# Performance work log

Measured on AMD Instinct MI355X. Metric: run time of the kernel, lower is better.

The kernel has to match this reference:

```python
import jax, jax.numpy as jnp
import numpy as np

TEMPERATURE = 8.0  # sqrt(d_k) with d_k=64
NEG = -9e15        # matches torch zero_vec constant -9000000000000000.0


def setup_inputs() -> dict:
    key = jax.random.key(0)
    k1, k2, k3, k4 = jax.random.split(key, 4)
    a, b, N, d = 32, 4, 1024, 64  # a = nhead*b, nhead = 8
    q = jax.random.normal(k1, (a, N, d), dtype=jnp.float32)
    k = jax.random.normal(k2, (a, N, d), dtype=jnp.float32)
    v = jax.random.normal(k3, (a, N, d), dtype=jnp.float32)
    adj = jax.random.randint(k4, (b, N, N), 0, 2, dtype=jnp.int32)
    return {"q": q, "k": k, "v": v, "adj": adj}


def reference(q, k, v, adj):
    # q,k,v: [nhead*b, N, d]; adj: [b, N, N]
    a, N, d = v.shape
    b = adj.shape[0]
    nhead = a // b
    # scores: [a, N, N]
    attn = jnp.einsum('bnd,bmd->bnm', q, k) / jnp.asarray(TEMPERATURE, q.dtype)
    # 'local' focus: mask by adjacency, broadcast over heads (head-major layout
    # matches torch's adj.unsqueeze(0).repeat(nhead,1,1,1).view(-1,N,N))
    attn = attn.reshape(nhead, b, N, N)
    attn = jnp.where(adj[None] > 0, attn, jnp.asarray(NEG, attn.dtype))
    attn = attn.reshape(a, N, N)
    attn = jax.nn.softmax(attn, axis=2)
    # dropout p=0.0 -> identity
    output = jnp.einsum('bnm,bmd->bnd', attn, v)
    return (output, attn)
```

## Files before the change

kernel.cpp:

```cpp
#include <hip/hip_runtime.h>
#include <hip/hip_bf16.h>

#define A_TOT 32
#define SEQ 1024
#define DIM 64
#define NT 16
#define GSTRIDE 1056
#define TILEB (8 * GSTRIDE)

typedef __attribute__((ext_vector_type(8))) short short8;
typedef __attribute__((ext_vector_type(4))) float f32x4;
typedef unsigned long long u64;

static __device__ __forceinline__ unsigned pack2bf(float a, float b) {
    union { __hip_bfloat16 h[2]; unsigned u; } x;
    x.h[0] = __float2bfloat16(a);
    x.h[1] = __float2bfloat16(b);
    return x.u;
}

static __device__ __forceinline__ void gload_lds16(const void* g, void* l) {
    __builtin_amdgcn_global_load_lds(
        (const __attribute__((address_space(1))) unsigned*)g,
        (__attribute__((address_space(3))) unsigned*)l, 16, 0, 0);
}

static __device__ __forceinline__ short8 lds_frag(const unsigned char* tile,
                                                  int row, int chunk) {
    const int byte = (row >> 3) * GSTRIDE + (row & 7) * 128 +
                     ((chunk ^ (row & 7)) << 4);
    return *reinterpret_cast<const short8*>(tile + byte);
}

#define WAITBAR(N) do {                                          \
    asm volatile("s_waitcnt vmcnt(" #N ")" ::: "memory");        \
    __builtin_amdgcn_sched_barrier(0);                           \
    __builtin_amdgcn_s_barrier();                                \
    __builtin_amdgcn_sched_barrier(0);                           \
    asm volatile("" ::: "memory");                               \
} while (0)

__global__ void prepass_kernel(const float* __restrict__ q,
                               const float* __restrict__ k,
                               const float* __restrict__ v,
                               const int* __restrict__ adj,
                               __hip_bfloat16* __restrict__ qb,
                               __hip_bfloat16* __restrict__ kb,
                               __hip_bfloat16* __restrict__ vt,
                               u64* __restrict__ adjm) {
    __shared__ __hip_bfloat16 tile[64][65];
    const int tid = threadIdx.x;
    if (blockIdx.y < 2) {
        const float* src = blockIdx.y ? k : q;
        __hip_bfloat16* dst = blockIdx.y ? kb : qb;
        int i = (blockIdx.x * 256 + tid) * 4;
        float4 f = *reinterpret_cast<const float4*>(src + i);
        union { __hip_bfloat16 h[4]; ushort4 u; } cv;
        cv.h[0] = __float2bfloat16(f.x);
        cv.h[1] = __float2bfloat16(f.y);
        cv.h[2] = __float2bfloat16(f.z);
        cv.h[3] = __float2bfloat16(f.w);
        *reinterpret_cast<ushort4*>(dst + i) = cv.u;
        return;
    }
    if (blockIdx.x < 512) {
        const int bh = blockIdx.x >> 4;
        const int n0 = (blockIdx.x & 15) * 64;
        const float* vsrc = v + ((size_t)bh * SEQ + n0) * DIM;
        for (int e = tid; e < 64 * 64; e += 256) {
            int i = e >> 6;
            int d = e & 63;
            tile[i][d] = __float2bfloat16(vsrc[(size_t)i * DIM + d]);
        }
        __syncthreads();
        __hip_bfloat16* vdst = vt + (size_t)bh * DIM * SEQ + n0;
        for (int e = tid; e < 64 * 64; e += 256) {
            int d = e >> 6;
            int i = e & 63;
            vdst[(size_t)d * SEQ + i] = tile[i][d];
        }
        return;
    }
    if (blockIdx.x < 1536) {
        const int px   = blockIdx.x - 512;
        const int wv   = tid >> 6;
        const int lane = tid & 63;
        const int wbase = px * 64 + wv * 16;
        for (int it = 0; it < 16; ++it) {
            const int w = wbase + it;
            const int a = adj[(size_t)w * 64 + lane];
            u64 m = __ballot(a > 0);
            if (lane == 0) adjm[w] = m;
        }
    }
}

__launch_bounds__(256)
__global__ void graph_attn_kernel(const __hip_bfloat16* __restrict__ qb,
                                  const __hip_bfloat16* __restrict__ kb,
                                  const __hip_bfloat16* __restrict__ vt,
                                  const u64* __restrict__ adjm,
                                  float* __restrict__ out,
                                  float* __restrict__ attn) {
    __shared__ __align__(16) unsigned char kstage[2][TILEB];
    __shared__ __align__(16) unsigned char vstage[2][TILEB];
    __shared__ float part[4][4][16];
    __shared__ float lsum_sh[4][16];

    const int wg    = (blockIdx.x & 7) * 64 + (blockIdx.x >> 3);
    const int bh    = wg >> 4;
    const int rb    = wg & 15;
    const int batch = bh & 3;
    const int tid   = threadIdx.x;
    const int wid   = tid >> 6;
    const int lane  = tid & 63;
    const int lr    = lane & 15;
    const int lgi   = lane >> 4;
    const int row16 = rb * 64 + wid * 16;

    const int sub  = lane >> 3;
    const int csrc = (lane & 7) ^ sub;

    const __hip_bfloat16* qrow = qb + ((size_t)bh * SEQ + row16 + lr) * DIM + lgi * 8;
    const short8 qf0 = *reinterpret_cast<const short8*>(qrow);
    const short8 qf1 = *reinterpret_cast<const short8*>(qrow + 32);

    const u64* mrow = adjm + ((size_t)batch * SEQ + row16 + lr) * (SEQ / 64);
    const __hip_bfloat16* kbh = kb + (size_t)bh * SEQ * DIM;
    const __hip_bfloat16* vth = vt + (size_t)bh * DIM * SEQ;

    const int kperm = (lr >> 2) * 8 + (lr & 3);

    auto stageK = [&](int t, int b) {
        const __hip_bfloat16* g0 = kbh + (size_t)(t * 64 + wid * 16) * DIM;
        unsigned char* l0 = &kstage[b][(wid * 2) * GSTRIDE];
        gload_lds16(g0 + (size_t)sub * DIM + csrc * 8, l0);
        gload_lds16(g0 + (size_t)(8 + sub) * DIM + csrc * 8, l0 + GSTRIDE);
    };
    auto stageV = [&](int t, int b) {
        const __hip_bfloat16* g0 = vth + (size_t)(wid * 16) * SEQ + t * 64;
        unsigned char* l0 = &vstage[b][(wid * 2) * GSTRIDE];
        gload_lds16(g0 + (size_t)sub * SEQ + csrc * 8, l0);
        gload_lds16(g0 + (size_t)(8 + sub) * SEQ + csrc * 8, l0 + GSTRIDE);
    };

    u64 mb = mrow[0], mn_ = 0;
    stageK(0, 0);
    WAITBAR(0);

    float lp = 0.f;
    int cur = 0;
    for (int t = 0; t < NT; ++t) {
        if (t < NT - 1) {
            mn_ = mrow[t + 1];
            stageK(t + 1, cur ^ 1);
        }
#pragma unroll
        for (int c = 0; c < 4; ++c) {
            const int cb = (c >> 1) * 32 + (c & 1) * 4;
            const int krow = cb + kperm;
            short8 kf0 = lds_frag(kstage[cur], krow, lgi);
            short8 kf1 = lds_frag(kstage[cur], krow, 4 + lgi);
            f32x4 acc = {0.f, 0.f, 0.f, 0.f};
            acc = __builtin_amdgcn_mfma_f32_16x16x32_bf16(kf0, qf0, acc, 0, 0, 0);
            acc = __builtin_amdgcn_mfma_f32_16x16x32_bf16(kf1, qf1, acc, 0, 0, 0);
            const unsigned b4 = (unsigned)(mb >> (cb + lgi * 8)) & 0xFu;
            float p0 = (b4 & 1u) ? __expf(acc[0] * 0.125f) : 0.f;
            float p1 = (b4 & 2u) ? __expf(acc[1] * 0.125f) : 0.f;
            float p2 = (b4 & 4u) ? __expf(acc[2] * 0.125f) : 0.f;
            float p3 = (b4 & 8u) ? __expf(acc[3] * 0.125f) : 0.f;
            lp += (p0 + p1) + (p2 + p3);
        }
        if (t < NT - 1) {
            mb = mn_;
            WAITBAR(0);
        }
        cur ^= 1;
    }

    part[wid][lgi][lr] = lp;
    asm volatile("" ::: "memory");
    if (lane < 16) {
        lsum_sh[wid][lane] = part[wid][0][lane] + part[wid][1][lane] +
                             part[wid][2][lane] + part[wid][3][lane];
    }
    __syncthreads();
    const float linv = 1.0f / (lsum_sh[wid][lr] + 1e-37f);

    f32x4 o[4];
#pragma unroll
    for (int c = 0; c < 4; ++c) o[c] = (f32x4){0.f, 0.f, 0.f, 0.f};

    mb = mrow[0];
    stageK(0, 0); stageV(0, 0);
    WAITBAR(0);

    float* attn_row = attn + (size_t)bh * SEQ * SEQ + (size_t)(row16 + lr) * SEQ;
    unsigned pk[4][2];
    cur = 0;
    for (int t = 0; t < NT; ++t) {
        if (t < NT - 1) {
            mn_ = mrow[t + 1];
            stageK(t + 1, cur ^ 1);
            stageV(t + 1, cur ^ 1);
        }
#pragma unroll
        for (int c = 0; c < 4; ++c) {
            const int cb = (c >> 1) * 32 + (c & 1) * 4;
            const int krow = cb + kperm;
            short8 kf0 = lds_frag(kstage[cur], krow, lgi);
            short8 kf1 = lds_frag(kstage[cur], krow, 4 + lgi);
            f32x4 acc = {0.f, 0.f, 0.f, 0.f};
            acc = __builtin_amdgcn_mfma_f32_16x16x32_bf16(kf0, qf0, acc, 0, 0, 0);
            acc = __builtin_amdgcn_mfma_f32_16x16x32_bf16(kf1, qf1, acc, 0, 0, 0);
            const unsigned b4 = (unsigned)(mb >> (cb + lgi * 8)) & 0xFu;
            float p0 = (b4 & 1u) ? __expf(acc[0] * 0.125f) * linv : 0.f;
            float p1 = (b4 & 2u) ? __expf(acc[1] * 0.125f) * linv : 0.f;
            float p2 = (b4 & 4u) ? __expf(acc[2] * 0.125f) * linv : 0.f;
            float p3 = (b4 & 8u) ? __expf(acc[3] * 0.125f) * linv : 0.f;
            pk[c][0] = pack2bf(p0, p1);
            pk[c][1] = pack2bf(p2, p3);
        }
#pragma unroll
        for (int c = 0; c < 4; ++c) {
            const int cb = (c >> 1) * 32 + (c & 1) * 4;
            const unsigned u01 = pk[c][0];
            const unsigned u23 = pk[c][1];
            float f0 = __uint_as_float(u01 << 16);
            float f1 = __uint_as_float(u01 & 0xffff0000u);
            float f2 = __uint_as_float(u23 << 16);
            float f3 = __uint_as_float(u23 & 0xffff0000u);
            *reinterpret_cast<float4*>(attn_row + t * 64 + cb + lgi * 8) =
                (float4){f0, f1, f2, f3};
        }
        union { unsigned u[4]; short8 s; } pf0, pf1;
        pf0.u[0] = pk[0][0]; pf0.u[1] = pk[0][1];
        pf0.u[2] = pk[1][0]; pf0.u[3] = pk[1][1];
        pf1.u[0] = pk[2][0]; pf1.u[1] = pk[2][1];
        pf1.u[2] = pk[3][0]; pf1.u[3] = pk[3][1];
#pragma unroll
        for (int c2 = 0; c2 < 4; ++c2) {
            const int vrow = c2 * 16 + lr;
            short8 vf0 = lds_frag(vstage[cur], vrow, lgi);
            short8 vf1 = lds_frag(vstage[cur], vrow, 4 + lgi);
            o[c2] = __builtin_amdgcn_mfma_f32_16x16x32_bf16(pf0.s, vf0, o[c2], 0, 0, 0);
            o[c2] = __builtin_amdgcn_mfma_f32_16x16x32_bf16(pf1.s, vf1, o[c2], 0, 0, 0);
        }
        if (t < NT - 1) {
            mb = mn_;
            WAITBAR(4);
        }
        cur ^= 1;
    }

    float* ob = out + (size_t)bh * SEQ * DIM + (size_t)row16 * DIM;
#pragma unroll
    for (int c2 = 0; c2 < 4; ++c2)
#pragma unroll
        for (int j = 0; j < 4; ++j)
            ob[(size_t)(lgi * 4 + j) * DIM + c2 * 16 + lr] = o[c2][j];
}

extern "C" void kernel_launch(void* const* d_in, const int* in_sizes, int n_in,
                              void* d_out, int out_size, void* d_ws, size_t ws_size,
                              hipStream_t stream) {
    const float* q   = (const float*)d_in[0];
    const float* k   = (const float*)d_in[1];
    const float* v   = (const float*)d_in[2];
    const int*   adj = (const int*)d_in[3];

    float* out  = (float*)d_out;
    float* attn = out + (size_t)A_TOT * SEQ * DIM;

    __hip_bfloat16* qb = (__hip_bfloat16*)d_ws;
    __hip_bfloat16* kb = qb + (size_t)A_TOT * SEQ * DIM;
    __hip_bfloat16* vt = kb + (size_t)A_TOT * SEQ * DIM;
    u64* adjm = (u64*)(vt + (size_t)A_TOT * SEQ * DIM);

    prepass_kernel<<<dim3(2048, 3), 256, 0, stream>>>(q, k, v, adj, qb, kb, vt, adjm);
    graph_attn_kernel<<<512, 256, 0, stream>>>(qb, kb, vt, adjm, out, attn);
}
```

Measured before the change: 61.87 us.

## Split softmax row-sum pass into separate split-K kernel with more blocks

Moves the first pass, which computes the masked exp row sums, out of the main attention kernel into its own kernel. That kernel launches 2048 blocks, each covering a quarter of the key range, and writes partial sums to workspace. The main kernel reads and combines the four partials, then runs only the normalize/store/PV pass. Attention probabilities are now stored directly in fp32 instead of being rounded through bf16, and a scheduling barrier is added. The intent is to spread the sum pass over more parallel blocks, at the cost of an extra launch and workspace traffic.

```diff
diff --git a/kernel.cpp b/kernel.cpp
--- a/kernel.cpp
+++ b/kernel.cpp
@@ -96,20 +96,18 @@
 }
 
 __launch_bounds__(256)
-__global__ void graph_attn_kernel(const __hip_bfloat16* __restrict__ qb,
-                                  const __hip_bfloat16* __restrict__ kb,
-                                  const __hip_bfloat16* __restrict__ vt,
-                                  const u64* __restrict__ adjm,
-                                  float* __restrict__ out,
-                                  float* __restrict__ attn) {
+__global__ void lsum_kernel(const __hip_bfloat16* __restrict__ qb,
+                            const __hip_bfloat16* __restrict__ kb,
+                            const u64* __restrict__ adjm,
+                            float* __restrict__ lpart) {
     __shared__ __align__(16) unsigned char kstage[2][TILEB];
-    __shared__ __align__(16) unsigned char vstage[2][TILEB];
     __shared__ float part[4][4][16];
-    __shared__ float lsum_sh[4][16];
-
-    const int wg    = (blockIdx.x & 7) * 64 + (blockIdx.x >> 3);
-    const int bh    = wg >> 4;
-    const int rb    = wg & 15;
+
+    const int wg    = (blockIdx.x & 7) * 256 + (blockIdx.x >> 3);
+    const int bh    = wg >> 6;
+    const int lidx  = wg & 63;
+    const int rb    = lidx >> 2;
+    const int kq    = lidx & 3;
     const int batch = bh & 3;
     const int tid   = threadIdx.x;
     const int wid   = tid >> 6;
@@ -117,6 +115,7 @@
     const int lr    = lane & 15;
     const int lgi   = lane >> 4;
     const int row16 = rb * 64 + wid * 16;
+    const int t0    = kq * 4;
 
     const int sub  = lane >> 3;
     const int csrc = (lane & 7) ^ sub;
@@ -127,8 +126,6 @@
 
     const u64* mrow = adjm + ((size_t)batch * SEQ + row16 + lr) * (SEQ / 64);
     const __hip_bfloat16* kbh = kb + (size_t)bh * SEQ * DIM;
-    const __hip_bfloat16* vth = vt + (size_t)bh * DIM * SEQ;
-
     const int kperm = (lr >> 2) * 8 + (lr & 3);
 
     auto stageK = [&](int t, int b) {
@@ -137,21 +134,17 @@
         gload_lds16(g0 + (size_t)sub * DIM + csrc * 8, l0);
         gload_lds16(g0 + (size_t)(8 + sub) * DIM + csrc * 8, l0 + GSTRIDE);
     };
-    auto stageV = [&](int t, int b) {
-        const __hip_bfloat16* g0 = vth + (size_t)(wid * 16) * SEQ + t * 64;
-        unsigned char* l0 = &vstage[b][(wid * 2) * GSTRIDE];
-        gload_lds16(g0 + (size_t)sub * SEQ + csrc * 8, l0);
-        gload_lds16(g0 + (size_t)(8 + sub) * SEQ + csrc * 8, l0 + GSTRIDE);
-    };
-
-    u64 mb = mrow[0], mn_ = 0;
-    stageK(0, 0);
+
+    u64 mb = mrow[t0], mn_ = 0;
+    stageK(t0, 0);
     WAITBAR(0);
 
     float lp = 0.f;
     int cur = 0;
-    for (int t = 0; t < NT; ++t) {
-        if (t < NT - 1) {
+#pragma unroll
+    for (int i = 0; i < 4; ++i) {
+        const int t = t0 + i;
+        if (i < 3) {
             mn_ = mrow[t + 1];
             stageK(t + 1, cur ^ 1);
         }
@@ -171,7 +164,7 @@
             float p3 = (b4 & 8u) ? __expf(acc[3] * 0.125f) : 0.f;
             lp += (p0 + p1) + (p2 + p3);
         }
-        if (t < NT - 1) {
+        if (i < 3) {
             mb = mn_;
             WAITBAR(0);
         }
@@ -181,29 +174,86 @@
     part[wid][lgi][lr] = lp;
     asm volatile("" ::: "memory");
     if (lane < 16) {
-        lsum_sh[wid][lane] = part[wid][0][lane] + part[wid][1][lane] +
-                             part[wid][2][lane] + part[wid][3][lane];
-    }
-    __syncthreads();
-    const float linv = 1.0f / (lsum_sh[wid][lr] + 1e-37f);
-
-    f32x4 o[4];
-#pragma unroll
-    for (int c = 0; c < 4; ++c) o[c] = (f32x4){0.f, 0.f, 0.f, 0.f};
-
-    mb = mrow[0];
+        float s = part[wid][0][lane] + part[wid][1][lane] +
+                  part[wid][2][lane] + part[wid][3][lane];
+        lpart[((size_t)kq * A_TOT + bh) * SEQ + row16 + lane] = s;
+    }
+}
+
+__launch_bounds__(256)
+__global__ void graph_attn_kernel(const __hip_bfloat16* __restrict__ qb,
+                                  const __hip_bfloat16* __restrict__ kb,
+                                  const __hip_bfloat16* __restrict__ vt,
+                                  const u64* __restrict__ adjm,
+                                  const float* __restrict__ lpart,
+                                  float* __restrict__ out,
+                                  float* __restrict__ attn) {
+    __shared__ __align__(16) unsigned char kstage[2][TILEB];
+    __shared__ __align__(16) unsigned char vstage[2][TILEB];
+
+    const int wg    = (blockIdx.x & 7) * 64 + (blockIdx.x >> 3);
+    const int bh    = wg >> 4;
+    const int rb    = wg & 15;
+    const int batch = bh & 3;
+    const int tid   = threadIdx.x;
+    const int wid   = tid >> 6;
+    const int lane  = tid & 63;
+    const int lr    = lane & 15;
+    const int lgi   = lane >> 4;
+    const int row16 = rb * 64 + wid * 16;
+
+    const int sub  = lane >> 3;
+    const int csrc = (lane & 7) ^ sub;
+
+    const __hip_bfloat16* qrow = qb + ((size_t)bh * SEQ + row16 + lr) * DIM + lgi * 8;
+    const short8 qf0 = *reinterpret_cast<const short8*>(qrow);
+    const short8 qf1 = *reinterpret_cast<const short8*>(qrow + 32);
+
+    const u64* mrow = adjm + ((size_t)batch * SEQ + row16 + lr) * (SEQ / 64);
+    const __hip_bfloat16* kbh = kb + (size_t)bh * SEQ * DIM;
+    const __hip_bfloat16* vth = vt + (size_t)bh * DIM * SEQ;
+
+    const int kperm = (lr >> 2) * 8 + (lr & 3);
+
+    auto stageK = [&](int t, int b) {
+        const __hip_bfloat16* g0 = kbh + (size_t)(t * 64 + wid * 16) * DIM;
+        unsigned char* l0 = &kstage[b][(wid * 2) * GSTRIDE];
+        gload_lds16(g0 + (size_t)sub * DIM + csrc * 8, l0);
+        gload_lds16(g0 + (size_t)(8 + sub) * DIM + csrc * 8, l0 + GSTRIDE);
+    };
+    auto stageV = [&](int t, int b) {
+        const __hip_bfloat16* g0 = vth + (size_t)(wid * 16) * SEQ + t * 64;
+        unsigned char* l0 = &vstage[b][(wid * 2) * GSTRIDE];
+        gload_lds16(g0 + (size_t)sub * SEQ + csrc * 8, l0);
+        gload_lds16(g0 + (size_t)(8 + sub) * SEQ + csrc * 8, l0 + GSTRIDE);
+    };
+
+    const float* lpr = lpart + (size_t)bh * SEQ + row16 + lr;
+    const float a0 = lpr[0];
+    const float a1 = lpr[(size_t)A_TOT * SEQ];
+    const float a2 = lpr[(size_t)2 * A_TOT * SEQ];
+    const float a3 = lpr[(size_t)3 * A_TOT * SEQ];
+
+    u64 mb = mrow[0], mn_ = 0;
     stageK(0, 0); stageV(0, 0);
     WAITBAR(0);
 
+    const float linv = 1.0f / (((a0 + a1) + (a2 + a3)) + 1e-37f);
+
+    f32x4 o[4];
+#pragma unroll
+    for (int c = 0; c < 4; ++c) o[c] = (f32x4){0.f, 0.f, 0.f, 0.f};
+
     float* attn_row = attn + (size_t)bh * SEQ * SEQ + (size_t)(row16 + lr) * SEQ;
     unsigned pk[4][2];
-    cur = 0;
+    int cur = 0;
     for (int t = 0; t < NT; ++t) {
         if (t < NT - 1) {
             mn_ = mrow[t + 1];
             stageK(t + 1, cur ^ 1);
             stageV(t + 1, cur ^ 1);
         }
+        __builtin_amdgcn_sched_barrier(0);
 #pragma unroll
         for (int c = 0; c < 4; ++c) {
             const int cb = (c >> 1) * 32 + (c & 1) * 4;
@@ -218,20 +268,10 @@
             float p1 = (b4 & 2u) ? __expf(acc[1] * 0.125f) * linv : 0.f;
             float p2 = (b4 & 4u) ? __expf(acc[2] * 0.125f) * linv : 0.f;
             float p3 = (b4 & 8u) ? __expf(acc[3] * 0.125f) * linv : 0.f;
+            *reinterpret_cast<float4*>(attn_row + t * 64 + cb + lgi * 8) =
+                (float4){p0, p1, p2, p3};
             pk[c][0] = pack2bf(p0, p1);
             pk[c][1] = pack2bf(p2, p3);
-        }
-#pragma unroll
-        for (int c = 0; c < 4; ++c) {
-            const int cb = (c >> 1) * 32 + (c & 1) * 4;
-            const unsigned u01 = pk[c][0];
-            const unsigned u23 = pk[c][1];
-            float f0 = __uint_as_float(u01 << 16);
-            float f1 = __uint_as_float(u01 & 0xffff0000u);
-            float f2 = __uint_as_float(u23 << 16);
-            float f3 = __uint_as_float(u23 & 0xffff0000u);
-            *reinterpret_cast<float4*>(attn_row + t * 64 + cb + lgi * 8) =
-                (float4){f0, f1, f2, f3};
         }
         union { unsigned u[4]; short8 s; } pf0, pf1;
         pf0.u[0] = pk[0][0]; pf0.u[1] = pk[0][1];
@@ -276,7 +316,9 @@
     __hip_bfloat16* kb = qb + (size_t)A_TOT * SEQ * DIM;
     __hip_bfloat16* vt = kb + (size_t)A_TOT * SEQ * DIM;
     u64* adjm = (u64*)(vt + (size_t)A_TOT * SEQ * DIM);
+    float* lpart = (float*)(adjm + 4 * SEQ * (SEQ / 64));
 
     prepass_kernel<<<dim3(2048, 3), 256, 0, stream>>>(q, k, v, adj, qb, kb, vt, adjm);
-    graph_attn_kernel<<<512, 256, 0, stream>>>(qb, kb, vt, adjm, out, attn);
-}
+    lsum_kernel<<<2048, 256, 0, stream>>>(qb, kb, adjm, lpart);
+    graph_attn_kernel<<<512, 256, 0, stream>>>(qb, kb, vt, adjm, lpart, out, attn);
+}
```

Result: no change. 62.61 us (+1.2%).
